# Kernel tuning notes

Measured on AMD Instinct MI355X. Metric: run time of the kernel, lower is better.

Reference implementation:

```python
import jax, jax.numpy as jnp
import numpy as np

B, P, H, A = 256, 196, 1024, 512

def setup_inputs() -> dict:
    key = jax.random.key(0)
    ks = jax.random.split(key, 20)
    s = 1.0 / np.sqrt(H)
    sa = 1.0 / np.sqrt(A)
    return {
        "spatial_image": jax.random.normal(ks[0], (B, P, H), jnp.float32),
        "decoder_out": jax.random.normal(ks[1], (B, H), jnp.float32),
        "st": jax.random.normal(ks[2], (B, H), jnp.float32),
        "W_sen_aff": jax.random.uniform(ks[3], (H, H), jnp.float32, -s, s),
        "b_sen_aff": jax.random.uniform(ks[4], (H,), jnp.float32, -s, s),
        "W_sen_att": jax.random.uniform(ks[5], (H, A), jnp.float32, -s, s),
        "b_sen_att": jax.random.uniform(ks[6], (A,), jnp.float32, -s, s),
        "W_h_aff": jax.random.uniform(ks[7], (H, H), jnp.float32, -s, s),
        "b_h_aff": jax.random.uniform(ks[8], (H,), jnp.float32, -s, s),
        "W_h_att": jax.random.uniform(ks[9], (H, A), jnp.float32, -s, s),
        "b_h_att": jax.random.uniform(ks[10], (A,), jnp.float32, -s, s),
        "W_v_att": jax.random.uniform(ks[11], (H, A), jnp.float32, -s, s),
        "b_v_att": jax.random.uniform(ks[12], (A,), jnp.float32, -s, s),
        "W_alpha": jax.random.uniform(ks[13], (A, 1), jnp.float32, -sa, sa),
        "b_alpha": jax.random.uniform(ks[14], (1,), jnp.float32, -sa, sa),
        "W_ctx": jax.random.uniform(ks[15], (H, H), jnp.float32, -s, s),
        "b_ctx": jax.random.uniform(ks[16], (H,), jnp.float32, -s, s),
    }

def reference(spatial_image, decoder_out, st,
              W_sen_aff, b_sen_aff, W_sen_att, b_sen_att,
              W_h_aff, b_h_aff, W_h_att, b_h_att,
              W_v_att, b_v_att, W_alpha, b_alpha, W_ctx, b_ctx):
    # visual_attn: [B, P, A]
    visual_attn = jnp.einsum('bph,ha->bpa', spatial_image, W_v_att) + b_v_att
    # sentinel path: [B, H] -> relu affine -> [B, A]
    sentinel_affine = jax.nn.relu(st @ W_sen_aff + b_sen_aff)
    sentinel_attn = sentinel_affine @ W_sen_att + b_sen_att
    # hidden path: [B, H] -> tanh affine -> [B, A]
    hidden_affine = jnp.tanh(decoder_out @ W_h_aff + b_h_aff)
    hidden_attn = hidden_affine @ W_h_att + b_h_att
    # concat sentinel as an extra "pixel": [B, P+1, H] and [B, P+1, A]
    concat_features = jnp.concatenate([spatial_image, sentinel_affine[:, None, :]], axis=1)
    attended_features = jnp.concatenate([visual_attn, sentinel_attn[:, None, :]], axis=1)
    attention = jnp.tanh(attended_features + hidden_attn[:, None, :])  # [B, P+1, A]
    alpha = (jnp.einsum('bpa,ao->bpo', attention, W_alpha) + b_alpha)[..., 0]  # [B, P+1]
    att_weights = jax.nn.softmax(alpha, axis=1)
    context = jnp.einsum('bph,bp->bh', concat_features, att_weights)  # [B, H]
    beta_value = att_weights[:, -1:]  # [B, 1]
    out_l = jnp.tanh((context + hidden_affine) @ W_ctx + b_ctx)  # [B, H]
    return (out_l, att_weights, beta_value)
```

## Files before the change

### kernel.cpp

```cpp
#include <hip/hip_runtime.h>
#include <stdint.h>
#include <stddef.h>

typedef __attribute__((ext_vector_type(4))) float f32x4;
typedef __attribute__((ext_vector_type(8))) short short8;


static __device__ __forceinline__ int lds_off(int row, int k) {
    int slot = (k >> 3) ^ ((row >> 1) & 3);
    return (row << 6) + (slot << 4) + ((k & 7) << 1);
}

static __device__ __forceinline__ unsigned div196(unsigned g) {
    return (unsigned)(((unsigned long long)g * 85599ull) >> 24);
}

static __device__ __forceinline__ unsigned short f2bf(float f) {
    union { float f; unsigned u; } v; v.f = f;
    unsigned r = v.u + 0x7FFFu + ((v.u >> 16) & 1u);
    return (unsigned short)(r >> 16);
}

static __device__ __forceinline__ unsigned long long pack4bf(f32x4 a) {
    return  (unsigned long long)f2bf(a[0])
         | ((unsigned long long)f2bf(a[1]) << 16)
         | ((unsigned long long)f2bf(a[2]) << 32)
         | ((unsigned long long)f2bf(a[3]) << 48);
}

static __device__ __forceinline__ float tanh_fast(float x) {
    float xc = fminf(fmaxf(x, -9.f), 9.f);
    float e = __builtin_amdgcn_exp2f(xc * 2.885390081777927f);
    return (e - 1.f) * __builtin_amdgcn_rcpf(e + 1.f);
}

static __device__ __forceinline__ void gload_lds16(const void* g, void* l) {
    __builtin_amdgcn_global_load_lds(
        (const __attribute__((address_space(1))) unsigned int*)g,
        (__attribute__((address_space(3))) unsigned int*)l, 16, 0, 0);
}

__global__ __launch_bounds__(512, 2) void attn_alpha_kernel(
    const float* __restrict__ spatial,
    const unsigned short* __restrict__ WvT,
    const float* __restrict__ b_v_att,
    const float* __restrict__ hidden_attn,
    const float* __restrict__ W_alpha,
    float* __restrict__ alpha)
{
    __shared__ char sA[2][8192];
    __shared__ char sB[2][32768];
    __shared__ float alpha_s[128];
    const int tid = threadIdx.x;
    const int row0 = blockIdx.x << 7;
    if (tid < 128) alpha_s[tid] = 0.f;

    const int lane = tid & 63, w = tid >> 6;
    const int wr = w >> 2, wc = w & 3;
    const int lrow = lane & 15, lk = lane >> 4;

    const int arow = tid >> 3;
    const int acol = (tid & 7) << 2;
    const float* Ap = spatial + (size_t)(row0 + arow) * 1024 + acol;
    const int aoff0 = lds_off(arow, acol);
    const int aoff1 = lds_off(arow + 64, acol);

    const int kg = (lane & 3) ^ ((lane >> 3) & 3);
    const unsigned short* Bp = WvT + (size_t)((w << 4) + (lane >> 2)) * 1024 + (kg << 3);

    f32x4 acc[4][8];
    f32x4 z = {0.f, 0.f, 0.f, 0.f};
    #pragma unroll
    for (int m = 0; m < 4; ++m)
        #pragma unroll
        for (int n = 0; n < 8; ++n) acc[m][n] = z;

    {
        f32x4 a0 = *(const f32x4*)(Ap);
        f32x4 a1 = *(const f32x4*)(Ap + 64 * 1024);
        #pragma unroll
        for (int r = 0; r < 4; ++r)
            gload_lds16(Bp + ((size_t)r << 17), sB[0] + (r << 13) + (w << 10));
        *(unsigned long long*)(sA[0] + aoff0) = pack4bf(a0);
        *(unsigned long long*)(sA[0] + aoff1) = pack4bf(a1);
    }
    __syncthreads();

    int cur = 0;
    for (int ks = 0; ks < 32; ++ks) {
        const int nxt = cur ^ 1;
        f32x4 a0n, a1n;
        if (ks < 31) {
            const float* Apk = Ap + ((ks + 1) << 5);
            a0n = *(const f32x4*)(Apk);
            a1n = *(const f32x4*)(Apk + 64 * 1024);
            const unsigned short* Bpk = Bp + ((ks + 1) << 5);
            #pragma unroll
            for (int r = 0; r < 4; ++r)
                gload_lds16(Bpk + ((size_t)r << 17), sB[nxt] + (r << 13) + (w << 10));
        }
        short8 af[4], bf[8];
        #pragma unroll
        for (int m = 0; m < 4; ++m)
            af[m] = *(const short8*)(sA[cur] + lds_off((wr << 6) + (m << 4) + lrow, lk << 3));
        #pragma unroll
        for (int n = 0; n < 8; ++n)
            bf[n] = *(const short8*)(sB[cur] + lds_off((wc << 7) + (n << 4) + lrow, lk << 3));
        #pragma unroll
        for (int m = 0; m < 4; ++m)
            #pragma unroll
            for (int n = 0; n < 8; ++n)
                acc[m][n] = __builtin_amdgcn_mfma_f32_16x16x32_bf16(af[m], bf[n], acc[m][n], 0, 0, 0);
        if (ks < 31) {
            *(unsigned long long*)(sA[nxt] + aoff0) = pack4bf(a0n);
            *(unsigned long long*)(sA[nxt] + aoff1) = pack4bf(a1n);
        }
        __syncthreads();
        cur = nxt;
    }

    const unsigned bb0 = div196((unsigned)row0);
    const unsigned bb1 = div196((unsigned)(row0 + 127));
    float bv[8], wa[8], h0[8], h1[8];
    #pragma unroll
    for (int n = 0; n < 8; ++n) {
        int g = (wc << 7) + (n << 4) + lrow;
        bv[n] = b_v_att[g];
        wa[n] = W_alpha[g];
        h0[n] = hidden_attn[bb0 * 512 + g];
        h1[n] = hidden_attn[bb1 * 512 + g];
    }
    #pragma unroll
    for (int m = 0; m < 4; ++m) {
        int rloc = (wr << 6) + (m << 4) + (lk << 2);
        #pragma unroll
        for (int i = 0; i < 4; ++i) {
            unsigned g = (unsigned)(row0 + rloc + i);
            bool first = (div196(g) == bb0);
            float s = 0.f;
            #pragma unroll
            for (int n = 0; n < 8; ++n) {
                float v = tanh_fast(acc[m][n][i] + bv[n] + (first ? h0[n] : h1[n]));
                s += v * wa[n];
            }
            #pragma unroll
            for (int off = 1; off < 16; off <<= 1) s += __shfl_xor(s, off);
            if (lrow == 0) atomicAdd(&alpha_s[rloc + i], s);
        }
    }
    __syncthreads();
    if (tid < 128) {
        unsigned g = (unsigned)(row0 + tid);
        unsigned bb = div196(g);
        unsigned p = g - bb * 196;
        alpha[bb * 196 + p] = alpha_s[tid];
    }
}

static __device__ __forceinline__ void mfma_tile_kloop(
    const float* __restrict__ Abase,
    const unsigned short* __restrict__ Bbase,
    char* sA, char* sB, f32x4 acc[4][4], int tid)
{
    const int lane = tid & 63;
    const int w = tid >> 6;
    const int wr = w >> 1, wc = w & 1;
    const int lrow = lane & 15, lk = lane >> 4;

    f32x4 z = {0.f, 0.f, 0.f, 0.f};
    #pragma unroll
    for (int m = 0; m < 4; ++m)
        #pragma unroll
        for (int n = 0; n < 4; ++n) acc[m][n] = z;

    for (int ks = 0; ks < 32; ++ks) {
        const int k0 = ks << 5;
        f32x4 a4[4];
        #pragma unroll
        for (int r = 0; r < 4; ++r) {
            int q = tid + (r << 8);
            int ar = q >> 3, kc = (q & 7) << 2;
            a4[r] = *(const f32x4*)(Abase + (size_t)ar * 1024 + k0 + kc);
        }
        short8 b8[2];
        #pragma unroll
        for (int r = 0; r < 2; ++r) {
            int c = tid + (r << 8);
            int br = c >> 2, kc = (c & 3) << 3;
            b8[r] = *(const short8*)(Bbase + (size_t)br * 1024 + k0 + kc);
        }
        __syncthreads();
        #pragma unroll
        for (int r = 0; r < 4; ++r) {
            int q = tid + (r << 8);
            int ar = q >> 3, kc = (q & 7) << 2;
            *(unsigned long long*)(sA + lds_off(ar, kc)) = pack4bf(a4[r]);
        }
        #pragma unroll
        for (int r = 0; r < 2; ++r) {
            int c = tid + (r << 8);
            int br = c >> 2, kc = (c & 3) << 3;
            *(short8*)(sB + lds_off(br, kc)) = b8[r];
        }
        __syncthreads();
        short8 af[4], bfr[4];
        #pragma unroll
        for (int m = 0; m < 4; ++m)
            af[m] = *(const short8*)(sA + lds_off((wr << 6) + (m << 4) + lrow, lk << 3));
        #pragma unroll
        for (int n = 0; n < 4; ++n)
            bfr[n] = *(const short8*)(sB + lds_off((wc << 6) + (n << 4) + lrow, lk << 3));
        #pragma unroll
        for (int m = 0; m < 4; ++m)
            #pragma unroll
            for (int n = 0; n < 4; ++n)
                acc[m][n] = __builtin_amdgcn_mfma_f32_16x16x32_bf16(af[m], bfr[n], acc[m][n], 0, 0, 0);
    }
}

struct GemmDesc { const float* A; const unsigned short* BT; const float* bias; float* C; int N; int act; };
struct GemmPair { GemmDesc d[2]; };

__global__ __launch_bounds__(256, 2) void gemm_pair_kernel(GemmPair p)
{
    GemmDesc d = p.d[blockIdx.z];
    __shared__ char sA[8192];
    __shared__ char sB[8192];
    const int tid = threadIdx.x;
    const int row0 = blockIdx.x << 7;
    const int col0 = blockIdx.y << 7;
    f32x4 acc[4][4];
    mfma_tile_kloop(d.A + (size_t)row0 * 1024, d.BT + (size_t)col0 * 1024, sA, sB, acc, tid);
    const int lane = tid & 63, w = tid >> 6;
    const int wr = w >> 1, wc = w & 1;
    const int lrow = lane & 15, lk = lane >> 4;
    #pragma unroll
    for (int n = 0; n < 4; ++n) {
        int col = col0 + (wc << 6) + (n << 4) + lrow;
        float bs = d.bias[col];
        #pragma unroll
        for (int m = 0; m < 4; ++m) {
            int rbase = row0 + (wr << 6) + (m << 4) + (lk << 2);
            #pragma unroll
            for (int i = 0; i < 4; ++i) {
                float v = acc[m][n][i] + bs;
                if (d.act == 1) v = fmaxf(v, 0.f);
                if (d.act == 2) v = tanh_fast(v);
                d.C[(size_t)(rbase + i) * d.N + col] = v;
            }
        }
    }
}

struct TransDesc { const float* src; unsigned short* dst; int K; int N; };
struct TransArgs { TransDesc d[6]; };

__global__ void transpose_cvt_kernel(TransArgs args) {
    TransDesc d = args.d[blockIdx.y];
    int nt = d.N >> 5;
    int tiles = (d.K >> 5) * nt;
    if ((int)blockIdx.x >= tiles) return;
    int tk = blockIdx.x / nt, tn = blockIdx.x % nt;
    __shared__ unsigned short tile[32][33];
    int tx = threadIdx.x & 31, ty = threadIdx.x >> 5;
    int k0 = tk << 5, n0 = tn << 5;
    #pragma unroll
    for (int j = 0; j < 4; ++j)
        tile[ty + j * 8][tx] = f2bf(d.src[(size_t)(k0 + ty + j * 8) * d.N + n0 + tx]);
    __syncthreads();
    #pragma unroll
    for (int j = 0; j < 4; ++j)
        d.dst[(size_t)(n0 + ty + j * 8) * d.K + k0 + tx] = tile[tx][ty + j * 8];
}

__global__ void softmax_sentinel_kernel(
    const float* __restrict__ alphab,
    const float* __restrict__ sen_att, const float* __restrict__ hid_att,
    const float* __restrict__ W_alpha,
    float* __restrict__ att, float* __restrict__ beta)
{
    int b = blockIdx.x, tid = threadIdx.x;
    __shared__ float al[197];
    __shared__ float red[4];
    if (tid < 196) al[tid] = alphab[b * 196 + tid];
    float s = 0.f;
    for (int a = tid; a < 512; a += 256)
        s += tanh_fast(sen_att[b * 512 + a] + hid_att[b * 512 + a]) * W_alpha[a];
    #pragma unroll
    for (int off = 1; off < 64; off <<= 1) s += __shfl_xor(s, off);
    if ((tid & 63) == 0) red[tid >> 6] = s;
    __syncthreads();
    if (tid == 0) al[196] = red[0] + red[1] + red[2] + red[3];
    __syncthreads();
    if (tid < 64) {
        float v[4];
        float mx = -1e30f;
        #pragma unroll
        for (int j = 0; j < 4; ++j) {
            int i = tid + j * 64;
            v[j] = (i < 197) ? al[i] : -1e30f;
            mx = fmaxf(mx, v[j]);
        }
        #pragma unroll
        for (int off = 1; off < 64; off <<= 1) mx = fmaxf(mx, __shfl_xor(mx, off));
        float sm = 0.f;
        #pragma unroll
        for (int j = 0; j < 4; ++j) {
            v[j] = __builtin_amdgcn_exp2f((v[j] - mx) * 1.442695040888963f);
            if (tid + j * 64 >= 197) v[j] = 0.f;
            sm += v[j];
        }
        #pragma unroll
        for (int off = 1; off < 64; off <<= 1) sm += __shfl_xor(sm, off);
        float inv = 1.f / sm;
        #pragma unroll
        for (int j = 0; j < 4; ++j) {
            int i = tid + j * 64;
            if (i < 197) {
                float wv = v[j] * inv;
                att[b * 197 + i] = wv;
                if (i == 196) beta[b] = wv;
            }
        }
    }
}

__global__ __launch_bounds__(256) void context_kernel(
    const float* __restrict__ spatial, const float* __restrict__ sen_aff,
    const float* __restrict__ hid_aff, const float* __restrict__ att,
    float* __restrict__ ctxh)
{
    int b = blockIdx.x, half = blockIdx.y, t = threadIdx.x;
    __shared__ float wsm[197];
    if (t < 197) wsm[t] = att[b * 197 + t];
    __syncthreads();
    int h2 = (half << 8) + t;
    const float2* sp = (const float2*)(spatial + (size_t)b * 196 * 1024) + h2;
    float ax = 0.f, ay = 0.f;
    #pragma unroll 4
    for (int p = 0; p < 196; ++p) {
        float2 x = sp[(size_t)p * 512];
        ax += wsm[p] * x.x; ay += wsm[p] * x.y;
    }
    float w196 = wsm[196];
    float2 sa = ((const float2*)(sen_aff + (size_t)b * 1024))[h2];
    float2 ha = ((const float2*)(hid_aff + (size_t)b * 1024))[h2];
    ctxh[(size_t)b * 1024 + 2 * h2]     = ax + w196 * sa.x + ha.x;
    ctxh[(size_t)b * 1024 + 2 * h2 + 1] = ay + w196 * sa.y + ha.y;
}

extern "C" void kernel_launch(void* const* d_in, const int* in_sizes, int n_in,
                              void* d_out, int out_size, void* d_ws, size_t ws_size,
                              hipStream_t stream)
{
    const float* spatial   = (const float*)d_in[0];
    const float* decoder   = (const float*)d_in[1];
    const float* st        = (const float*)d_in[2];
    const float* W_sen_aff = (const float*)d_in[3];
    const float* b_sen_aff = (const float*)d_in[4];
    const float* W_sen_att = (const float*)d_in[5];
    const float* b_sen_att = (const float*)d_in[6];
    const float* W_h_aff   = (const float*)d_in[7];
    const float* b_h_aff   = (const float*)d_in[8];
    const float* W_h_att   = (const float*)d_in[9];
    const float* b_h_att   = (const float*)d_in[10];
    const float* W_v_att   = (const float*)d_in[11];
    const float* b_v_att   = (const float*)d_in[12];
    const float* W_alpha   = (const float*)d_in[13];
    const float* W_ctx     = (const float*)d_in[15];
    const float* b_ctx     = (const float*)d_in[16];

    char* ws = (char*)d_ws;
    size_t off = 0;
    auto alloc = [&](size_t bytes) {
        char* p = ws + off; off += (bytes + 255) & ~(size_t)255; return p;
    };
    unsigned short* WvT  = (unsigned short*)alloc((size_t)512 * 1024 * 2);
    unsigned short* WsaT = (unsigned short*)alloc((size_t)1024 * 1024 * 2);
    unsigned short* WstT = (unsigned short*)alloc((size_t)512 * 1024 * 2);
    unsigned short* WhaT = (unsigned short*)alloc((size_t)1024 * 1024 * 2);
    unsigned short* WhtT = (unsigned short*)alloc((size_t)512 * 1024 * 2);
    unsigned short* WcxT = (unsigned short*)alloc((size_t)1024 * 1024 * 2);
    float* sen_aff = (float*)alloc((size_t)256 * 1024 * 4);
    float* sen_att = (float*)alloc((size_t)256 * 512 * 4);
    float* hid_aff = (float*)alloc((size_t)256 * 1024 * 4);
    float* hid_att = (float*)alloc((size_t)256 * 512 * 4);
    float* alphab  = (float*)alloc((size_t)256 * 196 * 4);
    float* ctxh    = (float*)alloc((size_t)256 * 1024 * 4);

    float* out_l    = (float*)d_out;
    float* out_att  = out_l + 256 * 1024;
    float* out_beta = out_att + 256 * 197;

    TransArgs ta;
    ta.d[0] = { W_v_att,   WvT,  1024, 512  };
    ta.d[1] = { W_sen_aff, WsaT, 1024, 1024 };
    ta.d[2] = { W_sen_att, WstT, 1024, 512  };
    ta.d[3] = { W_h_aff,   WhaT, 1024, 1024 };
    ta.d[4] = { W_h_att,   WhtT, 1024, 512  };
    ta.d[5] = { W_ctx,     WcxT, 1024, 1024 };
    transpose_cvt_kernel<<<dim3(1024, 6), 256, 0, stream>>>(ta);

    GemmPair p1;
    p1.d[0] = { st,      WsaT, b_sen_aff, sen_aff, 1024, 1 };
    p1.d[1] = { decoder, WhaT, b_h_aff,   hid_aff, 1024, 2 };
    gemm_pair_kernel<<<dim3(2, 8, 2), 256, 0, stream>>>(p1);

    GemmPair p2;
    p2.d[0] = { sen_aff, WstT, b_sen_att, sen_att, 512, 0 };
    p2.d[1] = { hid_aff, WhtT, b_h_att,   hid_att, 512, 0 };
    gemm_pair_kernel<<<dim3(2, 4, 2), 256, 0, stream>>>(p2);

    attn_alpha_kernel<<<392, 512, 0, stream>>>(spatial, WvT, b_v_att, hid_att, W_alpha, alphab);
    softmax_sentinel_kernel<<<256, 256, 0, stream>>>(alphab, sen_att, hid_att, W_alpha, out_att, out_beta);
    context_kernel<<<dim3(256, 2), 256, 0, stream>>>(spatial, sen_aff, hid_aff, out_att, ctxh);

    GemmPair p3;
    p3.d[0] = { ctxh, WcxT, b_ctx, out_l, 1024, 2 };
    p3.d[1] = { ctxh, WcxT, b_ctx, out_l, 1024, 2 };
    gemm_pair_kernel<<<dim3(2, 8, 1), 256, 0, stream>>>(p3);
}
```

Baseline: 246.8 us.

## Split attention GEMM over N into four column tiles and double-buffer small GEMMs

The main attention-alpha kernel moves from 128x512 tiles with 512 threads to 128x128 tiles with 256 threads, launching 1568 blocks instead of 392. Each block writes a partial alpha sum for its column slice, and the softmax kernel adds the four partials. A shared double-buffered k-loop with direct global-to-LDS loads for B is reused by the small GEMM kernels, which previously used a single-buffered loop. The aim is better occupancy and latency hiding. The cost is that the fp32 spatial input is re-read four times, once per column tile, which adds memory traffic.

Result: no change. 248.2 us (+0.6%).

```diff
diff --git a/kernel.cpp b/kernel.cpp
--- a/kernel.cpp
+++ b/kernel.cpp
@@ -4,6 +4,8 @@
 
 typedef __attribute__((ext_vector_type(4))) float f32x4;
 typedef __attribute__((ext_vector_type(8))) short short8;
+
+#define MROWS 50176
 
 
 static __device__ __forceinline__ int lds_off(int row, int k) {
@@ -40,91 +42,119 @@
         (__attribute__((address_space(3))) unsigned int*)l, 16, 0, 0);
 }
 
-__global__ __launch_bounds__(512, 2) void attn_alpha_kernel(
+static __device__ __forceinline__ void kloop_dbuf(
+    const float* __restrict__ Abase,
+    const unsigned short* __restrict__ Bbase,
+    char* sA0, char* sA1, char* sB0, char* sB1,
+    f32x4 acc[4][4], int tid)
+{
+    const int lane = tid & 63, w = tid >> 6;
+    const int lrow = lane & 15, lk = lane >> 4;
+    const int wr = w >> 1, wc = w & 1;
+
+    const float* Ap[4];
+    int aoff[4];
+    #pragma unroll
+    for (int r = 0; r < 4; ++r) {
+        int q = tid + (r << 8);
+        int ar = q >> 3, kc = (q & 7) << 2;
+        Ap[r] = Abase + (size_t)ar * 1024 + kc;
+        aoff[r] = lds_off(ar, kc);
+    }
+    const unsigned short* Bp[2];
+    int bdst[2];
+    #pragma unroll
+    for (int c = 0; c < 2; ++c) {
+        int ch = (w << 1) + c;
+        int row = (ch << 4) + (lane >> 2);
+        int kg = (lane & 3) ^ ((row >> 1) & 3);
+        Bp[c] = Bbase + (size_t)row * 1024 + (kg << 3);
+        bdst[c] = ch << 10;
+    }
+
+    f32x4 z = {0.f, 0.f, 0.f, 0.f};
+    #pragma unroll
+    for (int m = 0; m < 4; ++m)
+        #pragma unroll
+        for (int n = 0; n < 4; ++n) acc[m][n] = z;
+
+    {
+        f32x4 a[4];
+        #pragma unroll
+        for (int r = 0; r < 4; ++r) a[r] = *(const f32x4*)Ap[r];
+        #pragma unroll
+        for (int c = 0; c < 2; ++c) gload_lds16(Bp[c], sB0 + bdst[c]);
+        #pragma unroll
+        for (int r = 0; r < 4; ++r)
+            *(unsigned long long*)(sA0 + aoff[r]) = pack4bf(a[r]);
+    }
+    __syncthreads();
+
+    char* sAc = sA0; char* sAn = sA1;
+    char* sBc = sB0; char* sBn = sB1;
+    for (int ks = 0; ks < 32; ++ks) {
+        f32x4 an[4];
+        if (ks < 31) {
+            const int ko = (ks + 1) << 5;
+            #pragma unroll
+            for (int r = 0; r < 4; ++r) an[r] = *(const f32x4*)(Ap[r] + ko);
+            #pragma unroll
+            for (int c = 0; c < 2; ++c) gload_lds16(Bp[c] + ko, sBn + bdst[c]);
+        }
+        short8 af[4], bf[4];
+        #pragma unroll
+        for (int m = 0; m < 4; ++m)
+            af[m] = *(const short8*)(sAc + lds_off((wr << 6) + (m << 4) + lrow, lk << 3));
+        #pragma unroll
+        for (int n = 0; n < 4; ++n)
+            bf[n] = *(const short8*)(sBc + lds_off((wc << 6) + (n << 4) + lrow, lk << 3));
+        #pragma unroll
+        for (int m = 0; m < 4; ++m)
+            #pragma unroll
+            for (int n = 0; n < 4; ++n)
+                acc[m][n] = __builtin_amdgcn_mfma_f32_16x16x32_bf16(af[m], bf[n], acc[m][n], 0, 0, 0);
+        if (ks < 31) {
+            #pragma unroll
+            for (int r = 0; r < 4; ++r)
+                *(unsigned long long*)(sAn + aoff[r]) = pack4bf(an[r]);
+        }
+        __syncthreads();
+        char* t;
+        t = sAc; sAc = sAn; sAn = t;
+        t = sBc; sBc = sBn; sBn = t;
+    }
+}
+
+__global__ __launch_bounds__(256, 4) void attn_alpha_kernel(
     const float* __restrict__ spatial,
     const unsigned short* __restrict__ WvT,
     const float* __restrict__ b_v_att,
     const float* __restrict__ hidden_attn,
     const float* __restrict__ W_alpha,
-    float* __restrict__ alpha)
+    float* __restrict__ alphap)
 {
     __shared__ char sA[2][8192];
-    __shared__ char sB[2][32768];
+    __shared__ char sB[2][8192];
     __shared__ float alpha_s[128];
     const int tid = threadIdx.x;
-    const int row0 = blockIdx.x << 7;
+    const int n4 = blockIdx.x & 3, mt = blockIdx.x >> 2;
+    const int row0 = mt << 7, col0 = n4 << 7;
     if (tid < 128) alpha_s[tid] = 0.f;
 
+    f32x4 acc[4][4];
+    kloop_dbuf(spatial + (size_t)row0 * 1024, WvT + (size_t)col0 * 1024,
+               sA[0], sA[1], sB[0], sB[1], acc, tid);
+
     const int lane = tid & 63, w = tid >> 6;
-    const int wr = w >> 2, wc = w & 3;
+    const int wr = w >> 1, wc = w & 1;
     const int lrow = lane & 15, lk = lane >> 4;
-
-    const int arow = tid >> 3;
-    const int acol = (tid & 7) << 2;
-    const float* Ap = spatial + (size_t)(row0 + arow) * 1024 + acol;
-    const int aoff0 = lds_off(arow, acol);
-    const int aoff1 = lds_off(arow + 64, acol);
-
-    const int kg = (lane & 3) ^ ((lane >> 3) & 3);
-    const unsigned short* Bp = WvT + (size_t)((w << 4) + (lane >> 2)) * 1024 + (kg << 3);
-
-    f32x4 acc[4][8];
-    f32x4 z = {0.f, 0.f, 0.f, 0.f};
-    #pragma unroll
-    for (int m = 0; m < 4; ++m)
-        #pragma unroll
-        for (int n = 0; n < 8; ++n) acc[m][n] = z;
-
-    {
-        f32x4 a0 = *(const f32x4*)(Ap);
-        f32x4 a1 = *(const f32x4*)(Ap + 64 * 1024);
-        #pragma unroll
-        for (int r = 0; r < 4; ++r)
-            gload_lds16(Bp + ((size_t)r << 17), sB[0] + (r << 13) + (w << 10));
-        *(unsigned long long*)(sA[0] + aoff0) = pack4bf(a0);
-        *(unsigned long long*)(sA[0] + aoff1) = pack4bf(a1);
-    }
-    __syncthreads();
-
-    int cur = 0;
-    for (int ks = 0; ks < 32; ++ks) {
-        const int nxt = cur ^ 1;
-        f32x4 a0n, a1n;
-        if (ks < 31) {
-            const float* Apk = Ap + ((ks + 1) << 5);
-            a0n = *(const f32x4*)(Apk);
-            a1n = *(const f32x4*)(Apk + 64 * 1024);
-            const unsigned short* Bpk = Bp + ((ks + 1) << 5);
-            #pragma unroll
-            for (int r = 0; r < 4; ++r)
-                gload_lds16(Bpk + ((size_t)r << 17), sB[nxt] + (r << 13) + (w << 10));
-        }
-        short8 af[4], bf[8];
-        #pragma unroll
-        for (int m = 0; m < 4; ++m)
-            af[m] = *(const short8*)(sA[cur] + lds_off((wr << 6) + (m << 4) + lrow, lk << 3));
-        #pragma unroll
-        for (int n = 0; n < 8; ++n)
-            bf[n] = *(const short8*)(sB[cur] + lds_off((wc << 7) + (n << 4) + lrow, lk << 3));
-        #pragma unroll
-        for (int m = 0; m < 4; ++m)
-            #pragma unroll
-            for (int n = 0; n < 8; ++n)
-                acc[m][n] = __builtin_amdgcn_mfma_f32_16x16x32_bf16(af[m], bf[n], acc[m][n], 0, 0, 0);
-        if (ks < 31) {
-            *(unsigned long long*)(sA[nxt] + aoff0) = pack4bf(a0n);
-            *(unsigned long long*)(sA[nxt] + aoff1) = pack4bf(a1n);
-        }
-        __syncthreads();
-        cur = nxt;
-    }
 
     const unsigned bb0 = div196((unsigned)row0);
     const unsigned bb1 = div196((unsigned)(row0 + 127));
-    float bv[8], wa[8], h0[8], h1[8];
-    #pragma unroll
-    for (int n = 0; n < 8; ++n) {
-        int g = (wc << 7) + (n << 4) + lrow;
+    float bv[4], wa[4], h0[4], h1[4];
+    #pragma unroll
+    for (int n = 0; n < 4; ++n) {
+        int g = col0 + (wc << 6) + (n << 4) + lrow;
         bv[n] = b_v_att[g];
         wa[n] = W_alpha[g];
         h0[n] = hidden_attn[bb0 * 512 + g];
@@ -132,105 +162,40 @@
     }
     #pragma unroll
     for (int m = 0; m < 4; ++m) {
-        int rloc = (wr << 6) + (m << 4) + (lk << 2);
         #pragma unroll
         for (int i = 0; i < 4; ++i) {
-            unsigned g = (unsigned)(row0 + rloc + i);
-            bool first = (div196(g) == bb0);
+            int rloc = (wr << 6) + (m << 4) + (lk << 2) + i;
+            bool first = (div196((unsigned)(row0 + rloc)) == bb0);
             float s = 0.f;
             #pragma unroll
-            for (int n = 0; n < 8; ++n) {
+            for (int n = 0; n < 4; ++n) {
                 float v = tanh_fast(acc[m][n][i] + bv[n] + (first ? h0[n] : h1[n]));
                 s += v * wa[n];
             }
             #pragma unroll
             for (int off = 1; off < 16; off <<= 1) s += __shfl_xor(s, off);
-            if (lrow == 0) atomicAdd(&alpha_s[rloc + i], s);
-        }
-    }
-    __syncthreads();
-    if (tid < 128) {
-        unsigned g = (unsigned)(row0 + tid);
-        unsigned bb = div196(g);
-        unsigned p = g - bb * 196;
-        alpha[bb * 196 + p] = alpha_s[tid];
-    }
-}
-
-static __device__ __forceinline__ void mfma_tile_kloop(
-    const float* __restrict__ Abase,
-    const unsigned short* __restrict__ Bbase,
-    char* sA, char* sB, f32x4 acc[4][4], int tid)
-{
-    const int lane = tid & 63;
-    const int w = tid >> 6;
-    const int wr = w >> 1, wc = w & 1;
-    const int lrow = lane & 15, lk = lane >> 4;
-
-    f32x4 z = {0.f, 0.f, 0.f, 0.f};
-    #pragma unroll
-    for (int m = 0; m < 4; ++m)
-        #pragma unroll
-        for (int n = 0; n < 4; ++n) acc[m][n] = z;
-
-    for (int ks = 0; ks < 32; ++ks) {
-        const int k0 = ks << 5;
-        f32x4 a4[4];
-        #pragma unroll
-        for (int r = 0; r < 4; ++r) {
-            int q = tid + (r << 8);
-            int ar = q >> 3, kc = (q & 7) << 2;
-            a4[r] = *(const f32x4*)(Abase + (size_t)ar * 1024 + k0 + kc);
-        }
-        short8 b8[2];
-        #pragma unroll
-        for (int r = 0; r < 2; ++r) {
-            int c = tid + (r << 8);
-            int br = c >> 2, kc = (c & 3) << 3;
-            b8[r] = *(const short8*)(Bbase + (size_t)br * 1024 + k0 + kc);
-        }
-        __syncthreads();
-        #pragma unroll
-        for (int r = 0; r < 4; ++r) {
-            int q = tid + (r << 8);
-            int ar = q >> 3, kc = (q & 7) << 2;
-            *(unsigned long long*)(sA + lds_off(ar, kc)) = pack4bf(a4[r]);
-        }
-        #pragma unroll
-        for (int r = 0; r < 2; ++r) {
-            int c = tid + (r << 8);
-            int br = c >> 2, kc = (c & 3) << 3;
-            *(short8*)(sB + lds_off(br, kc)) = b8[r];
-        }
-        __syncthreads();
-        short8 af[4], bfr[4];
-        #pragma unroll
-        for (int m = 0; m < 4; ++m)
-            af[m] = *(const short8*)(sA + lds_off((wr << 6) + (m << 4) + lrow, lk << 3));
-        #pragma unroll
-        for (int n = 0; n < 4; ++n)
-            bfr[n] = *(const short8*)(sB + lds_off((wc << 6) + (n << 4) + lrow, lk << 3));
-        #pragma unroll
-        for (int m = 0; m < 4; ++m)
-            #pragma unroll
-            for (int n = 0; n < 4; ++n)
-                acc[m][n] = __builtin_amdgcn_mfma_f32_16x16x32_bf16(af[m], bfr[n], acc[m][n], 0, 0, 0);
-    }
+            if (lrow == 0) atomicAdd(&alpha_s[rloc], s);
+        }
+    }
+    __syncthreads();
+    if (tid < 128)
+        alphap[(size_t)n4 * MROWS + row0 + tid] = alpha_s[tid];
 }
 
 struct GemmDesc { const float* A; const unsigned short* BT; const float* bias; float* C; int N; int act; };
 struct GemmPair { GemmDesc d[2]; };
 
-__global__ __launch_bounds__(256, 2) void gemm_pair_kernel(GemmPair p)
+__global__ __launch_bounds__(256, 4) void gemm_pair_kernel(GemmPair p)
 {
     GemmDesc d = p.d[blockIdx.z];
-    __shared__ char sA[8192];
-    __shared__ char sB[8192];
+    __shared__ char sA[2][8192];
+    __shared__ char sB[2][8192];
     const int tid = threadIdx.x;
     const int row0 = blockIdx.x << 7;
     const int col0 = blockIdx.y << 7;
     f32x4 acc[4][4];
-    mfma_tile_kloop(d.A + (size_t)row0 * 1024, d.BT + (size_t)col0 * 1024, sA, sB, acc, tid);
+    kloop_dbuf(d.A + (size_t)row0 * 1024, d.BT + (size_t)col0 * 1024,
+               sA[0], sA[1], sB[0], sB[1], acc, tid);
     const int lane = tid & 63, w = tid >> 6;
     const int wr = w >> 1, wc = w & 1;
     const int lrow = lane & 15, lk = lane >> 4;
@@ -274,7 +239,7 @@
 }
 
 __global__ void softmax_sentinel_kernel(
-    const float* __restrict__ alphab,
+    const float* __restrict__ alphap,
     const float* __restrict__ sen_att, const float* __restrict__ hid_att,
     const float* __restrict__ W_alpha,
     float* __restrict__ att, float* __restrict__ beta)
@@ -282,7 +247,10 @@
     int b = blockIdx.x, tid = threadIdx.x;
     __shared__ float al[197];
     __shared__ float red[4];
-    if (tid < 196) al[tid] = alphab[b * 196 + tid];
+    if (tid < 196) {
+        size_t g = (size_t)b * 196 + tid;
+        al[tid] = alphap[g] + alphap[MROWS + g] + alphap[2 * MROWS + g] + alphap[3 * MROWS + g];
+    }
     float s = 0.f;
     for (int a = tid; a < 512; a += 256)
         s += tanh_fast(sen_att[b * 512 + a] + hid_att[b * 512 + a]) * W_alpha[a];
@@ -385,7 +353,7 @@
     float* sen_att = (float*)alloc((size_t)256 * 512 * 4);
     float* hid_aff = (float*)alloc((size_t)256 * 1024 * 4);
     float* hid_att = (float*)alloc((size_t)256 * 512 * 4);
-    float* alphab  = (float*)alloc((size_t)256 * 196 * 4);
+    float* alphap  = (float*)alloc((size_t)4 * MROWS * 4);
     float* ctxh    = (float*)alloc((size_t)256 * 1024 * 4);
 
     float* out_l    = (float*)d_out;
@@ -411,8 +379,8 @@
     p2.d[1] = { hid_aff, WhtT, b_h_att,   hid_att, 512, 0 };
     gemm_pair_kernel<<<dim3(2, 4, 2), 256, 0, stream>>>(p2);
 
-    attn_alpha_kernel<<<392, 512, 0, stream>>>(spatial, WvT, b_v_att, hid_att, W_alpha, alphab);
-    softmax_sentinel_kernel<<<256, 256, 0, stream>>>(alphab, sen_att, hid_att, W_alpha, out_att, out_beta);
+    attn_alpha_kernel<<<1568, 256, 0, stream>>>(spatial, WvT, b_v_att, hid_att, W_alpha, alphap);
+    softmax_sentinel_kernel<<<256, 256, 0, stream>>>(alphap, sen_att, hid_att, W_alpha, out_att, out_beta);
     context_kernel<<<dim3(256, 2), 256, 0, stream>>>(spatial, sen_aff, hid_aff, out_att, ctxh);
 
     GemmPair p3;
```
